# Kernel tuning notes

Hardware: AMD Instinct MI355X
Metric: run time of the kernel (lower is better)

Reference implementation:

```python
import jax, jax.numpy as jnp
import numpy as np

B, N_ST, N_SUB, WIN = 32, 8, 256, 2048


def setup_inputs() -> dict:
    key = jax.random.key(0)
    k1, k2 = jax.random.split(key)
    sel = jax.random.randint(k1, (B, WIN), 0, N_ST)
    schedule = jax.nn.one_hot(sel, N_ST, dtype=jnp.float32)
    # CSI: [B, n_stations, n_subcarriers, window]
    csi = jax.random.normal(k2, (B, N_ST, N_SUB, WIN), dtype=jnp.float32)
    return {"schedule": schedule, "csi": csi}


def reference(schedule, csi):
    # mask[b,t,s,w] = schedule[b,w,t]; out[b,s,w] = sum_t csi[b,t,s,w] * schedule[b,w,t]
    out = jnp.einsum('btsw,bwt->bsw', csi, schedule)
    return jnp.transpose(out, (0, 2, 1))
```

## Files before the change

### kernel.cpp

```cpp
#include <hip/hip_runtime.h>

constexpr int B     = 32;
constexpr int N_ST  = 8;
constexpr int N_SUB = 256;
constexpr int WIN   = 2048;

constexpr int TW  = 64;
constexpr int TS  = 64;
constexpr int PAD = 65;

__global__ __launch_bounds__(256)
void station_agg_kernel(const float* __restrict__ schedule,
                        const float* __restrict__ csi,
                        float* __restrict__ out)
{
    __shared__ float sched_t[N_ST][TW];
    __shared__ float tile[TW * PAD];

    const int s0 = blockIdx.x * TS;
    const int w0 = blockIdx.y * TW;
    const int b  = blockIdx.z;
    const int k  = threadIdx.x;

    {
        const float* sp = schedule + ((size_t)b * WIN + w0) * N_ST;
        const int e0 = k * 2;
        const float2 v = *(const float2*)(sp + e0);
        sched_t[e0 & 7][e0 >> 3]         = v.x;
        sched_t[(e0 + 1) & 7][(e0 + 1) >> 3] = v.y;
    }
    __syncthreads();

    const int w4   = k & 15;
    const int srow = k >> 4;

    float4 acc[4];
#pragma unroll
    for (int m = 0; m < 4; ++m) acc[m] = make_float4(0.f, 0.f, 0.f, 0.f);

    const size_t base_b = (size_t)b * N_ST * N_SUB * WIN;
#pragma unroll
    for (int t = 0; t < N_ST; ++t) {
        const float4 sv = *(const float4*)&sched_t[t][w4 * 4];
        const float* cp = csi + base_b
                        + ((size_t)t * N_SUB + (s0 + srow)) * WIN
                        + (w0 + w4 * 4);
#pragma unroll
        for (int m = 0; m < 4; ++m) {
            const float4 c = *(const float4*)(cp + (size_t)(16 * m) * WIN);
            acc[m].x += c.x * sv.x;
            acc[m].y += c.y * sv.y;
            acc[m].z += c.z * sv.z;
            acc[m].w += c.w * sv.w;
        }
    }

#pragma unroll
    for (int m = 0; m < 4; ++m) {
        const int s = srow + 16 * m;
        tile[(w4 * 4 + 0) * PAD + s] = acc[m].x;
        tile[(w4 * 4 + 1) * PAD + s] = acc[m].y;
        tile[(w4 * 4 + 2) * PAD + s] = acc[m].z;
        tile[(w4 * 4 + 3) * PAD + s] = acc[m].w;
    }
    __syncthreads();

    const int s4 = k & 15;
    const int wr = k >> 4;
#pragma unroll
    for (int m2 = 0; m2 < 4; ++m2) {
        const int w = wr + 16 * m2;
        float4 o;
        o.x = tile[w * PAD + s4 * 4 + 0];
        o.y = tile[w * PAD + s4 * 4 + 1];
        o.z = tile[w * PAD + s4 * 4 + 2];
        o.w = tile[w * PAD + s4 * 4 + 3];
        *(float4*)(out + ((size_t)b * WIN + (w0 + w)) * N_SUB + (s0 + s4 * 4)) = o;
    }
}

extern "C" void kernel_launch(void* const* d_in, const int* in_sizes, int n_in,
                              void* d_out, int out_size, void* d_ws, size_t ws_size,
                              hipStream_t stream) {
    const float* schedule = (const float*)d_in[0];
    const float* csi      = (const float*)d_in[1];
    float* out            = (float*)d_out;

    dim3 grid(N_SUB / TS, WIN / TW, B);
    dim3 block(256);
    station_agg_kernel<<<grid, block, 0, stream>>>(schedule, csi, out);
}
```

Before: 704.5 us.

## Reshape tiles to 256 window by 16 subcarriers with nontemporal loads and stores

Changes the block tile from 64x64 to 256 window positions by 16 subcarriers, so each wavefront reads one full contiguous 1 KB row segment per load. The shared-memory transpose is redone with a 260-float stride, and both global loads and stores use nontemporal builtins to avoid polluting the cache on this streaming workload. Output writes become 64-byte runs per window row instead of 256-byte runs, which may reduce write coalescing.

Result: faster. 669.8 us (-4.9%).

```diff
diff --git a/kernel.cpp b/kernel.cpp
--- a/kernel.cpp
+++ b/kernel.cpp
@@ -5,9 +5,11 @@
 constexpr int N_SUB = 256;
 constexpr int WIN   = 2048;
 
-constexpr int TW  = 64;
-constexpr int TS  = 64;
-constexpr int PAD = 65;
+constexpr int TW  = 256;
+constexpr int TS  = 16;
+constexpr int STR = 260;
+
+typedef float f4 __attribute__((ext_vector_type(4)));
 
 __global__ __launch_bounds__(256)
 void station_agg_kernel(const float* __restrict__ schedule,
@@ -15,67 +17,60 @@
                         float* __restrict__ out)
 {
     __shared__ float sched_t[N_ST][TW];
-    __shared__ float tile[TW * PAD];
+    __shared__ float tile2[TS * STR];
 
     const int s0 = blockIdx.x * TS;
     const int w0 = blockIdx.y * TW;
     const int b  = blockIdx.z;
     const int k  = threadIdx.x;
+    const int wv = k >> 6;
+    const int l  = k & 63;
 
     {
-        const float* sp = schedule + ((size_t)b * WIN + w0) * N_ST;
-        const int e0 = k * 2;
-        const float2 v = *(const float2*)(sp + e0);
-        sched_t[e0 & 7][e0 >> 3]         = v.x;
-        sched_t[(e0 + 1) & 7][(e0 + 1) >> 3] = v.y;
+        const float* sp = schedule + ((size_t)b * WIN + w0 + k) * N_ST;
+        const f4 a = *(const f4*)sp;
+        const f4 c = *(const f4*)(sp + 4);
+        sched_t[0][k] = a.x; sched_t[1][k] = a.y;
+        sched_t[2][k] = a.z; sched_t[3][k] = a.w;
+        sched_t[4][k] = c.x; sched_t[5][k] = c.y;
+        sched_t[6][k] = c.z; sched_t[7][k] = c.w;
     }
     __syncthreads();
 
-    const int w4   = k & 15;
-    const int srow = k >> 4;
+    f4 acc[4];
+#pragma unroll
+    for (int j = 0; j < 4; ++j) acc[j] = (f4)(0.0f);
 
-    float4 acc[4];
-#pragma unroll
-    for (int m = 0; m < 4; ++m) acc[m] = make_float4(0.f, 0.f, 0.f, 0.f);
-
-    const size_t base_b = (size_t)b * N_ST * N_SUB * WIN;
+    const size_t bbase = (size_t)b * N_ST * N_SUB * WIN;
 #pragma unroll
     for (int t = 0; t < N_ST; ++t) {
-        const float4 sv = *(const float4*)&sched_t[t][w4 * 4];
-        const float* cp = csi + base_b
-                        + ((size_t)t * N_SUB + (s0 + srow)) * WIN
-                        + (w0 + w4 * 4);
+        const f4 sv = *(const f4*)&sched_t[t][4 * l];
+        const float* cp = csi + bbase
+                        + ((size_t)t * N_SUB + (s0 + 4 * wv)) * WIN
+                        + (w0 + 4 * l);
 #pragma unroll
-        for (int m = 0; m < 4; ++m) {
-            const float4 c = *(const float4*)(cp + (size_t)(16 * m) * WIN);
-            acc[m].x += c.x * sv.x;
-            acc[m].y += c.y * sv.y;
-            acc[m].z += c.z * sv.z;
-            acc[m].w += c.w * sv.w;
+        for (int j = 0; j < 4; ++j) {
+            const f4 c = __builtin_nontemporal_load((const f4*)(cp + (size_t)j * WIN));
+            acc[j] += c * sv;
         }
     }
 
 #pragma unroll
-    for (int m = 0; m < 4; ++m) {
-        const int s = srow + 16 * m;
-        tile[(w4 * 4 + 0) * PAD + s] = acc[m].x;
-        tile[(w4 * 4 + 1) * PAD + s] = acc[m].y;
-        tile[(w4 * 4 + 2) * PAD + s] = acc[m].z;
-        tile[(w4 * 4 + 3) * PAD + s] = acc[m].w;
-    }
+    for (int j = 0; j < 4; ++j)
+        *(f4*)&tile2[(4 * wv + j) * STR + 4 * l] = acc[j];
     __syncthreads();
 
-    const int s4 = k & 15;
-    const int wr = k >> 4;
 #pragma unroll
-    for (int m2 = 0; m2 < 4; ++m2) {
-        const int w = wr + 16 * m2;
-        float4 o;
-        o.x = tile[w * PAD + s4 * 4 + 0];
-        o.y = tile[w * PAD + s4 * 4 + 1];
-        o.z = tile[w * PAD + s4 * 4 + 2];
-        o.w = tile[w * PAD + s4 * 4 + 3];
-        *(float4*)(out + ((size_t)b * WIN + (w0 + w)) * N_SUB + (s0 + s4 * 4)) = o;
+    for (int m = 0; m < 4; ++m) {
+        const int wrow = 16 * wv + (l >> 2) + 64 * m;
+        const int sl   = 4 * (l & 3);
+        f4 o;
+        o.x = tile2[(sl + 0) * STR + wrow];
+        o.y = tile2[(sl + 1) * STR + wrow];
+        o.z = tile2[(sl + 2) * STR + wrow];
+        o.w = tile2[(sl + 3) * STR + wrow];
+        __builtin_nontemporal_store(o,
+            (f4*)(out + ((size_t)b * WIN + (w0 + wrow)) * N_SUB + (s0 + sl)));
     }
 }
 
```
